# Optimization experiments

Measured on AMD Instinct MI355X. Metric: run time of the kernel, lower is better.

Reference implementation:

```python
import jax, jax.numpy as jnp
import numpy as np
import math

DIM = 256
HEADS = 8
DIM_HEAD = 64
INNER = HEADS * DIM_HEAD  # 512
WIN = 8
STRIDE = 4
W = 32          # patch_w_num
N = W * W       # 1024 tokens
B = 64
SCALE = DIM_HEAD ** -0.5


def setup_inputs() -> dict:
    key = jax.random.key(0)
    ks = jax.random.split(key, 6)
    return {
        "x": jax.random.normal(ks[0], (B, N, DIM), jnp.float32),
        "w_qkv": jax.random.normal(ks[1], (DIM, 3 * INNER), jnp.float32) * 0.02,
        "w_pro": jax.random.normal(ks[2], (3 * INNER, 3 * INNER), jnp.float32) * 0.02,
        "b_pro": jnp.zeros((3 * INNER,), jnp.float32),
        "w_out": jax.random.normal(ks[3], (INNER, DIM), jnp.float32) * 0.02,
        "b_out": jnp.zeros((DIM,), jnp.float32),
    }


def _window_ranges(stride):
    # Replicates window_split's static range construction (Python ints only).
    edges = list(range(-WIN, W + 1, WIN))
    pairs = list(zip(edges[:-1], edges[1:]))
    ranges = []
    for (i0, i1) in pairs:
        for (j0, j1) in pairs:
            r = [min(max(v + stride, 0), W) for v in (i0, j0, i1, j1)]
            if r[2] != r[0] and r[3] != r[1]:
                ranges.append(r)
    return ranges


def _cal_window(q, k, v, stride):
    # q,k,v: [b, h, n, d]
    b, h, n, d = q.shape
    ranges = _window_ranges(stride)
    S = WIN * WIN

    def split(t):
        t5 = t.reshape(b, h, W, W, d)
        blks = []
        for r0, c0, r1, c1 in ranges:
            blk = t5[:, :, r0:r1, c0:c1, :].reshape(b, h, -1, d)
            pad = S - blk.shape[2]
            blk = jnp.pad(blk, ((0, 0), (0, 0), (0, pad), (0, 0)))
            blks.append(blk)
        return jnp.stack(blks, axis=0)  # [nb, b, h, S, d]

    qs, ks_, vs = split(q), split(k), split(v)
    # NOTE: softmax runs over padded (zero) keys too, faithful to the source.
    dots = jnp.einsum('nbhid,nbhjd->nbhij', qs, ks_) * SCALE
    attn = jax.nn.softmax(dots, axis=-1)
    out = jnp.einsum('nbhij,nbhjd->nbhid', attn, vs)  # [nb, b, h, S, d]

    # window_merge: stitch variable-size blocks back into [b, h, W, W, d]
    h_count = int(math.sqrt(len(ranges)))
    rows = []
    for i in range(0, len(ranges), h_count):
        row = []
        for j in range(h_count):
            r0, c0, r1, c1 = ranges[i + j]
            num = (r1 - r0) * (c1 - c0)
            row.append(out[i + j, :, :, :num, :].reshape(b, h, r1 - r0, c1 - c0, d))
        rows.append(jnp.concatenate(row, axis=3))
    full = jnp.concatenate(rows, axis=2)  # [b, h, W, W, d]
    # 'b h num_h num_w d -> b (num_h num_w) (h d)'
    return full.transpose(0, 2, 3, 1, 4).reshape(b, W * W, h * d)


def reference(x, w_qkv, w_pro, b_pro, w_out, b_out):
    qkv = x @ w_qkv                                   # [b, n, 3*inner]
    qkv = jax.nn.gelu(qkv, approximate=False) @ w_pro + b_pro
    q, k, v = jnp.split(qkv, 3, axis=-1)

    def to_heads(t):
        bb, nn_ = t.shape[0], t.shape[1]
        return t.reshape(bb, nn_, HEADS, DIM_HEAD).transpose(0, 2, 1, 3)

    q, k, v = to_heads(q), to_heads(k), to_heads(v)
    outs = [_cal_window(q, k, v, s) for s in range(0, WIN, STRIDE)]
    out = jnp.mean(jnp.stack(outs, axis=-1), axis=-1)  # [b, n, inner]
    return out @ w_out + b_out
```

## Files before the change

### kernel.cpp

```cpp
#include <hip/hip_runtime.h>
#include <hip/hip_bf16.h>
#include <stdint.h>


#define TILE 64
#define BKK  32

typedef short bf16x8 __attribute__((ext_vector_type(8)));
typedef float f32x4 __attribute__((ext_vector_type(4)));

__device__ __forceinline__ unsigned short f2bf(float f) {
    unsigned u = __float_as_uint(f);
    return (unsigned short)((u + 0x7fffu + ((u >> 16) & 1u)) >> 16);
}

__device__ __forceinline__ float gelu_exact(float v) {
    return 0.5f * v * (1.0f + erff(v * 0.70710678118654752f));
}

__global__ __launch_bounds__(256) void conv_bf16(const float* __restrict__ src,
                                                 unsigned short* __restrict__ dst, int n4) {
    int i = blockIdx.x * 256 + threadIdx.x;
    const int stride = gridDim.x * 256;
    for (; i < n4; i += stride) {
        float4 v = reinterpret_cast<const float4*>(src)[i];
        ushort4 o;
        o.x = f2bf(v.x); o.y = f2bf(v.y); o.z = f2bf(v.z); o.w = f2bf(v.w);
        reinterpret_cast<ushort4*>(dst)[i] = o;
    }
}

__global__ __launch_bounds__(256) void transpose_bf16(const float* __restrict__ w,
                                                      unsigned short* __restrict__ wT,
                                                      int K, int N) {
    __shared__ float t[32][33];
    const int kb = blockIdx.y * 32, nb = blockIdx.x * 32;
    const int r = threadIdx.x >> 5, c = threadIdx.x & 31;
    #pragma unroll
    for (int i = 0; i < 4; ++i)
        t[r + i * 8][c] = w[(size_t)(kb + r + i * 8) * N + nb + c];
    __syncthreads();
    #pragma unroll
    for (int i = 0; i < 4; ++i)
        wT[(size_t)(nb + r + i * 8) * K + kb + c] = f2bf(t[c][r + i * 8]);
}

template<bool GELU, bool BIAS, bool OUTBF>
__global__ __launch_bounds__(256) void gemm_mfma(
    const unsigned short* __restrict__ A,
    const unsigned short* __restrict__ BT,
    const float* __restrict__ bias,
    void* __restrict__ Cv, int M, int N, int K, int nbx)
{
    __shared__ __align__(16) short lA[128 * BKK];
    __shared__ __align__(16) short lB[128 * BKK];
    const int tid  = threadIdx.x;
    const int lane = tid & 63;
    const int wid  = tid >> 6;

    const int cpx = gridDim.x >> 3;
    const int wg  = (blockIdx.x & 7) * cpx + (blockIdx.x >> 3);
    const int nb  = wg % nbx, mb = wg / nbx;

    const size_t bm = (size_t)mb * 128;
    const size_t bn = (size_t)nb * 128;

    const int wr = wid >> 1, wc = wid & 1;
    const int mr = wr * 64, nr = wc * 64;

    f32x4 acc[4][4] = {};

    const int srow = lane >> 2;
    const int sk8  = lane & 3;

    for (int k0 = 0; k0 < K; k0 += BKK) {
        #pragma unroll
        for (int s = 0; s < 2; ++s) {
            const int i = wid * 2 + s;
            const int row = i * 16 + srow;
            const unsigned short* ga = A  + (bm + row) * (size_t)K + k0 + sk8 * 8;
            const unsigned short* gb = BT + (bn + row) * (size_t)K + k0 + sk8 * 8;
            __builtin_amdgcn_global_load_lds(
                (const __attribute__((address_space(1))) unsigned int*)ga,
                (__attribute__((address_space(3))) unsigned int*)(lA + i * 512), 16, 0, 0);
            __builtin_amdgcn_global_load_lds(
                (const __attribute__((address_space(1))) unsigned int*)gb,
                (__attribute__((address_space(3))) unsigned int*)(lB + i * 512), 16, 0, 0);
        }
        __syncthreads();

        const int fr = lane & 15;
        const int fk = (lane >> 4) * 8;
        bf16x8 af[4], bq[4];
        #pragma unroll
        for (int m = 0; m < 4; ++m)
            af[m] = *reinterpret_cast<const bf16x8*>(&lA[(mr + m * 16 + fr) * BKK + fk]);
        #pragma unroll
        for (int n = 0; n < 4; ++n)
            bq[n] = *reinterpret_cast<const bf16x8*>(&lB[(nr + n * 16 + fr) * BKK + fk]);
        #pragma unroll
        for (int m = 0; m < 4; ++m)
            #pragma unroll
            for (int n = 0; n < 4; ++n)
                acc[m][n] = __builtin_amdgcn_mfma_f32_16x16x32_bf16(af[m], bq[n], acc[m][n], 0, 0, 0);
        __syncthreads();
    }

    const int fr = lane & 15;
    const int fq = lane >> 4;
    #pragma unroll
    for (int n = 0; n < 4; ++n) {
        const size_t col = bn + nr + n * 16 + fr;
        const float bv = BIAS ? bias[col] : 0.0f;
        #pragma unroll
        for (int m = 0; m < 4; ++m) {
            const size_t rbase = bm + mr + m * 16 + fq * 4;
            f32x4 a = acc[m][n];
            #pragma unroll
            for (int j = 0; j < 4; ++j) {
                float v = a[j] + bv;
                if (GELU) v = gelu_exact(v);
                if (OUTBF)
                    ((unsigned short*)Cv)[(rbase + j) * (size_t)N + col] = f2bf(v);
                else
                    ((float*)Cv)[(rbase + j) * (size_t)N + col] = v;
            }
        }
    }
}

template<bool GELU, bool BIAS, bool MEANA>
__global__ __launch_bounds__(256) void gemm_f32(
    const float* __restrict__ A, const float* __restrict__ A2,
    const float* __restrict__ B, const float* __restrict__ bias,
    float* __restrict__ C, int M, int N, int K)
{
    __shared__ __align__(16) float As[BKK][TILE + 4];
    __shared__ __align__(16) float Bs[BKK][TILE + 4];
    const int tid = threadIdx.x;
    const int tx = tid & 15;
    const int ty = tid >> 4;
    const long bm = (long)blockIdx.y * TILE;
    const long bn = (long)blockIdx.x * TILE;

    float acc[4][4] = {};

    for (int k0 = 0; k0 < K; k0 += BKK) {
        #pragma unroll
        for (int i = 0; i < 2; ++i) {
            int f4  = tid + i * 256;
            int row = f4 >> 3;
            int kk  = (f4 & 7) << 2;
            float4 a = *reinterpret_cast<const float4*>(A + (bm + row) * (long)K + k0 + kk);
            if (MEANA) {
                float4 a2 = *reinterpret_cast<const float4*>(A2 + (bm + row) * (long)K + k0 + kk);
                a.x = 0.5f * (a.x + a2.x); a.y = 0.5f * (a.y + a2.y);
                a.z = 0.5f * (a.z + a2.z); a.w = 0.5f * (a.w + a2.w);
            }
            As[kk + 0][row] = a.x; As[kk + 1][row] = a.y;
            As[kk + 2][row] = a.z; As[kk + 3][row] = a.w;
        }
        #pragma unroll
        for (int i = 0; i < 2; ++i) {
            int f4   = tid + i * 256;
            int krow = f4 >> 4;
            int nn   = (f4 & 15) << 2;
            *reinterpret_cast<float4*>(&Bs[krow][nn]) =
                *reinterpret_cast<const float4*>(B + (long)(k0 + krow) * N + bn + nn);
        }
        __syncthreads();
        #pragma unroll
        for (int kk = 0; kk < BKK; ++kk) {
            float4 av = *reinterpret_cast<const float4*>(&As[kk][ty << 2]);
            float4 bv = *reinterpret_cast<const float4*>(&Bs[kk][tx << 2]);
            float a_[4] = {av.x, av.y, av.z, av.w};
            float b_[4] = {bv.x, bv.y, bv.z, bv.w};
            #pragma unroll
            for (int u = 0; u < 4; ++u)
                #pragma unroll
                for (int w = 0; w < 4; ++w)
                    acc[u][w] = fmaf(a_[u], b_[w], acc[u][w]);
        }
        __syncthreads();
    }

    #pragma unroll
    for (int u = 0; u < 4; ++u) {
        long row = bm + (ty << 2) + u;
        float vals[4];
        #pragma unroll
        for (int w = 0; w < 4; ++w) {
            float v = acc[u][w];
            if (BIAS) v += bias[bn + (tx << 2) + w];
            if (GELU) v = gelu_exact(v);
            vals[w] = v;
        }
        *reinterpret_cast<float4*>(C + row * (long)N + bn + (tx << 2)) =
            make_float4(vals[0], vals[1], vals[2], vals[3]);
    }
}

__global__ __launch_bounds__(256) void attn_win(
    const float* __restrict__ qkvp, float* __restrict__ out0, float* __restrict__ out4)
{
    __shared__ __align__(16) float qT[64][68];
    __shared__ __align__(16) float kT[64][68];
    __shared__ __align__(16) float vS[64][68];
    __shared__ float pS[64][66];
    __shared__ float invS[64];

    const int widx = blockIdx.x;
    const int h    = blockIdx.y;
    const int b    = blockIdx.z;
    const int tid  = threadIdx.x;

    int r0, c0, nr, nc;
    float* outbuf;
    if (widx < 16) {
        r0 = (widx >> 2) << 3; c0 = (widx & 3) << 3;
        nr = 8; nc = 8;
        outbuf = out0;
    } else {
        int w  = widx - 16;
        int ri = w / 5, ci = w % 5;
        r0 = (ri == 0) ? 0 : (8 * ri - 4);
        nr = (ri == 0 || ri == 4) ? 4 : 8;
        c0 = (ci == 0) ? 0 : (8 * ci - 4);
        nc = (ci == 0 || ci == 4) ? 4 : 8;
        outbuf = out4;
    }
    const int num = nr * nc;
    const int ncl = (nc == 8) ? 3 : 2;
    const size_t tokbase = (size_t)b * 1024;

    for (int f4 = tid; f4 < num * 16; f4 += 256) {
        int t  = f4 >> 4;
        int d4 = (f4 & 15) << 2;
        int n  = ((r0 + (t >> ncl)) << 5) + c0 + (t & (nc - 1));
        const float* base = qkvp + (tokbase + n) * 1536 + h * 64 + d4;
        float4 qv = *reinterpret_cast<const float4*>(base);
        float4 kv = *reinterpret_cast<const float4*>(base + 512);
        float4 vv = *reinterpret_cast<const float4*>(base + 1024);
        qT[d4 + 0][t] = qv.x; qT[d4 + 1][t] = qv.y; qT[d4 + 2][t] = qv.z; qT[d4 + 3][t] = qv.w;
        kT[d4 + 0][t] = kv.x; kT[d4 + 1][t] = kv.y; kT[d4 + 2][t] = kv.z; kT[d4 + 3][t] = kv.w;
        *reinterpret_cast<float4*>(&vS[t][d4]) = vv;
    }
    __syncthreads();

    const int i0 = (tid >> 4) << 2;
    const int j0 = (tid & 15) << 2;
    if (i0 < num && j0 < num) {
        float acc[4][4] = {};
        #pragma unroll 16
        for (int d = 0; d < 64; ++d) {
            float4 qv = *reinterpret_cast<const float4*>(&qT[d][i0]);
            float4 kv = *reinterpret_cast<const float4*>(&kT[d][j0]);
            float q_[4] = {qv.x, qv.y, qv.z, qv.w};
            float k_[4] = {kv.x, kv.y, kv.z, kv.w};
            #pragma unroll
            for (int u = 0; u < 4; ++u)
                #pragma unroll
                for (int w = 0; w < 4; ++w)
                    acc[u][w] = fmaf(q_[u], k_[w], acc[u][w]);
        }
        #pragma unroll
        for (int u = 0; u < 4; ++u)
            #pragma unroll
            for (int w = 0; w < 4; ++w)
                pS[i0 + u][j0 + w] = acc[u][w] * 0.125f;
    }
    __syncthreads();

    if (tid < num) {
        const int i = tid;
        float m = (num < 64) ? 0.0f : -3.4e38f;
        for (int j = 0; j < num; ++j) m = fmaxf(m, pS[i][j]);
        float s = (float)(64 - num) * __expf(-m);
        for (int j = 0; j < num; ++j) {
            float e = __expf(pS[i][j] - m);
            pS[i][j] = e;
            s += e;
        }
        invS[i] = 1.0f / s;
    }
    __syncthreads();

    const int d0 = j0;
    if (i0 < num) {
        float acc[4][4] = {};
        #pragma unroll 8
        for (int j = 0; j < num; ++j) {
            float4 vv = *reinterpret_cast<const float4*>(&vS[j][d0]);
            float v_[4] = {vv.x, vv.y, vv.z, vv.w};
            float p_[4];
            #pragma unroll
            for (int u = 0; u < 4; ++u) p_[u] = pS[i0 + u][j];
            #pragma unroll
            for (int u = 0; u < 4; ++u)
                #pragma unroll
                for (int w = 0; w < 4; ++w)
                    acc[u][w] = fmaf(p_[u], v_[w], acc[u][w]);
        }
        #pragma unroll
        for (int u = 0; u < 4; ++u) {
            int t = i0 + u;
            int n = ((r0 + (t >> ncl)) << 5) + c0 + (t & (nc - 1));
            float inv = invS[t];
            *reinterpret_cast<float4*>(outbuf + (tokbase + n) * 512 + h * 64 + d0) =
                make_float4(acc[u][0] * inv, acc[u][1] * inv, acc[u][2] * inv, acc[u][3] * inv);
        }
    }
}

extern "C" void kernel_launch(void* const* d_in, const int* in_sizes, int n_in,
                              void* d_out, int out_size, void* d_ws, size_t ws_size,
                              hipStream_t stream) {
    const float* x     = (const float*)d_in[0];
    const float* w_qkv = (const float*)d_in[1];
    const float* w_pro = (const float*)d_in[2];
    const float* b_pro = (const float*)d_in[3];
    const float* w_out = (const float*)d_in[4];
    const float* b_out = (const float*)d_in[5];
    float* out = (float*)d_out;

    const int B = 64;
    const size_t WQKVT = 1536 * 256 * 2;
    const size_t WPROT = 1536 * 1536 * 2;
    const size_t PERB  = 1024 * (256 * 2 + 1536 * 2 + 1536 * 4 + 512 * 4 + 512 * 4);
    int CB = 16;
    while (CB > 1 && WQKVT + WPROT + (size_t)CB * PERB > ws_size) CB >>= 1;
    const int NCHUNK = B / CB;
    const int CM = CB * 1024;

    char* w8 = (char*)d_ws;
    unsigned short* wqkvT = (unsigned short*)w8;
    unsigned short* wproT = (unsigned short*)(w8 + WQKVT);
    char* cbase = w8 + WQKVT + WPROT;
    unsigned short* xb     = (unsigned short*)cbase;
    unsigned short* gelu_b = (unsigned short*)(cbase + (size_t)CM * 512);
    float*          qkvp   = (float*)(cbase + (size_t)CM * 512 + (size_t)CM * 3072);
    float*          att0   = (float*)((char*)qkvp + (size_t)CM * 6144);
    float*          att4   = (float*)((char*)att0 + (size_t)CM * 2048);

    dim3 blk(256);

    transpose_bf16<<<dim3(1536 / 32, 256 / 32), blk, 0, stream>>>(w_qkv, wqkvT, 256, 1536);
    transpose_bf16<<<dim3(1536 / 32, 1536 / 32), blk, 0, stream>>>(w_pro, wproT, 1536, 1536);

    const int nbx = 12;
    const int gg  = (CM / 128) * nbx;

    for (int c = 0; c < NCHUNK; ++c) {
        const size_t tok0 = (size_t)c * CM;
        conv_bf16<<<512, blk, 0, stream>>>(x + tok0 * 256, xb, CM * 256 / 4);
        gemm_mfma<true, false, true><<<gg, blk, 0, stream>>>(
            xb, wqkvT, nullptr, gelu_b, CM, 1536, 256, nbx);
        gemm_mfma<false, true, false><<<gg, blk, 0, stream>>>(
            gelu_b, wproT, b_pro, qkvp, CM, 1536, 1536, nbx);
        attn_win<<<dim3(41, 8, CB), blk, 0, stream>>>(qkvp, att0, att4);
        gemm_f32<false, true, true><<<dim3(256 / TILE, CM / TILE), blk, 0, stream>>>(
            att0, att4, w_out, b_out, out + tok0 * 256, CM, 256, 512);
    }
}
```

Before: 1.497 ms.

## Store qkv and attention outputs in bf16 and run output projection on MFMA

The pro-projection GEMM now writes bf16 instead of fp32, and the window-attention kernel reads bf16 and writes bf16 into one concatenated buffer holding both stride outputs. The mean of the two outputs is folded into a doubled, halved, transposed w_out (K=1024), so the final projection runs on the bf16 MFMA GEMM rather than the fp32 SIMT GEMM. This roughly halves intermediate memory traffic and moves the last GEMM onto matrix cores, at the cost of extra bf16 rounding on q/k/v and attention outputs.

After: 1.330 ms. -11.2%, faster.

```diff
diff --git a/kernel.cpp b/kernel.cpp
--- a/kernel.cpp
+++ b/kernel.cpp
@@ -3,8 +3,7 @@
 #include <stdint.h>
 
 
-#define TILE 64
-#define BKK  32
+#define BKK 32
 
 typedef short bf16x8 __attribute__((ext_vector_type(8)));
 typedef float f32x4 __attribute__((ext_vector_type(4)));
@@ -13,7 +12,9 @@
     unsigned u = __float_as_uint(f);
     return (unsigned short)((u + 0x7fffu + ((u >> 16) & 1u)) >> 16);
 }
-
+__device__ __forceinline__ float bf2f(unsigned short u) {
+    return __uint_as_float((unsigned)u << 16);
+}
 __device__ __forceinline__ float gelu_exact(float v) {
     return 0.5f * v * (1.0f + erff(v * 0.70710678118654752f));
 }
@@ -43,6 +44,24 @@
     #pragma unroll
     for (int i = 0; i < 4; ++i)
         wT[(size_t)(nb + r + i * 8) * K + kb + c] = f2bf(t[c][r + i * 8]);
+}
+
+__global__ __launch_bounds__(256) void make_w4T(const float* __restrict__ w,
+                                                unsigned short* __restrict__ w4T) {
+    __shared__ float t[32][33];
+    const int kb = blockIdx.y * 32, nb = blockIdx.x * 32;
+    const int r = threadIdx.x >> 5, c = threadIdx.x & 31;
+    #pragma unroll
+    for (int i = 0; i < 4; ++i)
+        t[r + i * 8][c] = w[(size_t)(kb + r + i * 8) * 256 + nb + c];
+    __syncthreads();
+    #pragma unroll
+    for (int i = 0; i < 4; ++i) {
+        unsigned short v = f2bf(0.5f * t[c][r + i * 8]);
+        size_t n = nb + r + i * 8, k = kb + c;
+        w4T[n * 1024 + k]       = v;
+        w4T[n * 1024 + 512 + k] = v;
+    }
 }
 
 template<bool GELU, bool BIAS, bool OUTBF>
@@ -129,79 +148,8 @@
     }
 }
 
-template<bool GELU, bool BIAS, bool MEANA>
-__global__ __launch_bounds__(256) void gemm_f32(
-    const float* __restrict__ A, const float* __restrict__ A2,
-    const float* __restrict__ B, const float* __restrict__ bias,
-    float* __restrict__ C, int M, int N, int K)
-{
-    __shared__ __align__(16) float As[BKK][TILE + 4];
-    __shared__ __align__(16) float Bs[BKK][TILE + 4];
-    const int tid = threadIdx.x;
-    const int tx = tid & 15;
-    const int ty = tid >> 4;
-    const long bm = (long)blockIdx.y * TILE;
-    const long bn = (long)blockIdx.x * TILE;
-
-    float acc[4][4] = {};
-
-    for (int k0 = 0; k0 < K; k0 += BKK) {
-        #pragma unroll
-        for (int i = 0; i < 2; ++i) {
-            int f4  = tid + i * 256;
-            int row = f4 >> 3;
-            int kk  = (f4 & 7) << 2;
-            float4 a = *reinterpret_cast<const float4*>(A + (bm + row) * (long)K + k0 + kk);
-            if (MEANA) {
-                float4 a2 = *reinterpret_cast<const float4*>(A2 + (bm + row) * (long)K + k0 + kk);
-                a.x = 0.5f * (a.x + a2.x); a.y = 0.5f * (a.y + a2.y);
-                a.z = 0.5f * (a.z + a2.z); a.w = 0.5f * (a.w + a2.w);
-            }
-            As[kk + 0][row] = a.x; As[kk + 1][row] = a.y;
-            As[kk + 2][row] = a.z; As[kk + 3][row] = a.w;
-        }
-        #pragma unroll
-        for (int i = 0; i < 2; ++i) {
-            int f4   = tid + i * 256;
-            int krow = f4 >> 4;
-            int nn   = (f4 & 15) << 2;
-            *reinterpret_cast<float4*>(&Bs[krow][nn]) =
-                *reinterpret_cast<const float4*>(B + (long)(k0 + krow) * N + bn + nn);
-        }
-        __syncthreads();
-        #pragma unroll
-        for (int kk = 0; kk < BKK; ++kk) {
-            float4 av = *reinterpret_cast<const float4*>(&As[kk][ty << 2]);
-            float4 bv = *reinterpret_cast<const float4*>(&Bs[kk][tx << 2]);
-            float a_[4] = {av.x, av.y, av.z, av.w};
-            float b_[4] = {bv.x, bv.y, bv.z, bv.w};
-            #pragma unroll
-            for (int u = 0; u < 4; ++u)
-                #pragma unroll
-                for (int w = 0; w < 4; ++w)
-                    acc[u][w] = fmaf(a_[u], b_[w], acc[u][w]);
-        }
-        __syncthreads();
-    }
-
-    #pragma unroll
-    for (int u = 0; u < 4; ++u) {
-        long row = bm + (ty << 2) + u;
-        float vals[4];
-        #pragma unroll
-        for (int w = 0; w < 4; ++w) {
-            float v = acc[u][w];
-            if (BIAS) v += bias[bn + (tx << 2) + w];
-            if (GELU) v = gelu_exact(v);
-            vals[w] = v;
-        }
-        *reinterpret_cast<float4*>(C + row * (long)N + bn + (tx << 2)) =
-            make_float4(vals[0], vals[1], vals[2], vals[3]);
-    }
-}
-
 __global__ __launch_bounds__(256) void attn_win(
-    const float* __restrict__ qkvp, float* __restrict__ out0, float* __restrict__ out4)
+    const unsigned short* __restrict__ qkvp, unsigned short* __restrict__ attc)
 {
     __shared__ __align__(16) float qT[64][68];
     __shared__ __align__(16) float kT[64][68];
@@ -214,12 +162,10 @@
     const int b    = blockIdx.z;
     const int tid  = threadIdx.x;
 
-    int r0, c0, nr, nc;
-    float* outbuf;
+    int r0, c0, nr, nc, sOff;
     if (widx < 16) {
         r0 = (widx >> 2) << 3; c0 = (widx & 3) << 3;
-        nr = 8; nc = 8;
-        outbuf = out0;
+        nr = 8; nc = 8; sOff = 0;
     } else {
         int w  = widx - 16;
         int ri = w / 5, ci = w % 5;
@@ -227,7 +173,7 @@
         nr = (ri == 0 || ri == 4) ? 4 : 8;
         c0 = (ci == 0) ? 0 : (8 * ci - 4);
         nc = (ci == 0 || ci == 4) ? 4 : 8;
-        outbuf = out4;
+        sOff = 512;
     }
     const int num = nr * nc;
     const int ncl = (nc == 8) ? 3 : 2;
@@ -237,13 +183,16 @@
         int t  = f4 >> 4;
         int d4 = (f4 & 15) << 2;
         int n  = ((r0 + (t >> ncl)) << 5) + c0 + (t & (nc - 1));
-        const float* base = qkvp + (tokbase + n) * 1536 + h * 64 + d4;
-        float4 qv = *reinterpret_cast<const float4*>(base);
-        float4 kv = *reinterpret_cast<const float4*>(base + 512);
-        float4 vv = *reinterpret_cast<const float4*>(base + 1024);
-        qT[d4 + 0][t] = qv.x; qT[d4 + 1][t] = qv.y; qT[d4 + 2][t] = qv.z; qT[d4 + 3][t] = qv.w;
-        kT[d4 + 0][t] = kv.x; kT[d4 + 1][t] = kv.y; kT[d4 + 2][t] = kv.z; kT[d4 + 3][t] = kv.w;
-        *reinterpret_cast<float4*>(&vS[t][d4]) = vv;
+        const unsigned short* base = qkvp + (tokbase + n) * 1536 + h * 64 + d4;
+        ushort4 qv = *reinterpret_cast<const ushort4*>(base);
+        ushort4 kv = *reinterpret_cast<const ushort4*>(base + 512);
+        ushort4 vv = *reinterpret_cast<const ushort4*>(base + 1024);
+        qT[d4 + 0][t] = bf2f(qv.x); qT[d4 + 1][t] = bf2f(qv.y);
+        qT[d4 + 2][t] = bf2f(qv.z); qT[d4 + 3][t] = bf2f(qv.w);
+        kT[d4 + 0][t] = bf2f(kv.x); kT[d4 + 1][t] = bf2f(kv.y);
+        kT[d4 + 2][t] = bf2f(kv.z); kT[d4 + 3][t] = bf2f(kv.w);
+        vS[t][d4 + 0] = bf2f(vv.x); vS[t][d4 + 1] = bf2f(vv.y);
+        vS[t][d4 + 2] = bf2f(vv.z); vS[t][d4 + 3] = bf2f(vv.w);
     }
     __syncthreads();
 
@@ -306,8 +255,10 @@
             int t = i0 + u;
             int n = ((r0 + (t >> ncl)) << 5) + c0 + (t & (nc - 1));
             float inv = invS[t];
-            *reinterpret_cast<float4*>(outbuf + (tokbase + n) * 512 + h * 64 + d0) =
-                make_float4(acc[u][0] * inv, acc[u][1] * inv, acc[u][2] * inv, acc[u][3] * inv);
+            ushort4 o;
+            o.x = f2bf(acc[u][0] * inv); o.y = f2bf(acc[u][1] * inv);
+            o.z = f2bf(acc[u][2] * inv); o.w = f2bf(acc[u][3] * inv);
+            *reinterpret_cast<ushort4*>(attc + (tokbase + n) * 1024 + sOff + h * 64 + d0) = o;
         }
     }
 }
@@ -326,39 +277,42 @@
     const int B = 64;
     const size_t WQKVT = 1536 * 256 * 2;
     const size_t WPROT = 1536 * 1536 * 2;
-    const size_t PERB  = 1024 * (256 * 2 + 1536 * 2 + 1536 * 4 + 512 * 4 + 512 * 4);
+    const size_t W4T   = 256 * 1024 * 2;
+    const size_t PERB  = 1024 * (256 * 2 + 1536 * 2 + 1536 * 2 + 1024 * 2);
     int CB = 16;
-    while (CB > 1 && WQKVT + WPROT + (size_t)CB * PERB > ws_size) CB >>= 1;
+    while (CB > 1 && WQKVT + WPROT + W4T + (size_t)CB * PERB > ws_size) CB >>= 1;
     const int NCHUNK = B / CB;
     const int CM = CB * 1024;
 
     char* w8 = (char*)d_ws;
     unsigned short* wqkvT = (unsigned short*)w8;
     unsigned short* wproT = (unsigned short*)(w8 + WQKVT);
-    char* cbase = w8 + WQKVT + WPROT;
+    unsigned short* w4T   = (unsigned short*)(w8 + WQKVT + WPROT);
+    char* cbase = w8 + WQKVT + WPROT + W4T;
     unsigned short* xb     = (unsigned short*)cbase;
     unsigned short* gelu_b = (unsigned short*)(cbase + (size_t)CM * 512);
-    float*          qkvp   = (float*)(cbase + (size_t)CM * 512 + (size_t)CM * 3072);
-    float*          att0   = (float*)((char*)qkvp + (size_t)CM * 6144);
-    float*          att4   = (float*)((char*)att0 + (size_t)CM * 2048);
+    unsigned short* qkvp_b = (unsigned short*)(cbase + (size_t)CM * 512 + (size_t)CM * 3072);
+    unsigned short* attc   = (unsigned short*)((char*)qkvp_b + (size_t)CM * 3072);
 
     dim3 blk(256);
 
     transpose_bf16<<<dim3(1536 / 32, 256 / 32), blk, 0, stream>>>(w_qkv, wqkvT, 256, 1536);
     transpose_bf16<<<dim3(1536 / 32, 1536 / 32), blk, 0, stream>>>(w_pro, wproT, 1536, 1536);
-
-    const int nbx = 12;
-    const int gg  = (CM / 128) * nbx;
+    make_w4T<<<dim3(256 / 32, 512 / 32), blk, 0, stream>>>(w_out, w4T);
+
+    const int nbx12 = 12;
+    const int gg    = (CM / 128) * nbx12;
+    const int gg4   = (CM / 128) * 2;
 
     for (int c = 0; c < NCHUNK; ++c) {
         const size_t tok0 = (size_t)c * CM;
         conv_bf16<<<512, blk, 0, stream>>>(x + tok0 * 256, xb, CM * 256 / 4);
         gemm_mfma<true, false, true><<<gg, blk, 0, stream>>>(
-            xb, wqkvT, nullptr, gelu_b, CM, 1536, 256, nbx);
-        gemm_mfma<false, true, false><<<gg, blk, 0, stream>>>(
-            gelu_b, wproT, b_pro, qkvp, CM, 1536, 1536, nbx);
-        attn_win<<<dim3(41, 8, CB), blk, 0, stream>>>(qkvp, att0, att4);
-        gemm_f32<false, true, true><<<dim3(256 / TILE, CM / TILE), blk, 0, stream>>>(
-            att0, att4, w_out, b_out, out + tok0 * 256, CM, 256, 512);
-    }
-}
+            xb, wqkvT, nullptr, gelu_b, CM, 1536, 256, nbx12);
+        gemm_mfma<false, true, true><<<gg, blk, 0, stream>>>(
+            gelu_b, wproT, b_pro, qkvp_b, CM, 1536, 1536, nbx12);
+        attn_win<<<dim3(41, 8, CB), blk, 0, stream>>>(qkvp_b, attc);
+        gemm_mfma<false, true, false><<<gg4, blk, 0, stream>>>(
+            attc, w4T, b_out, out + tok0 * 256, CM, 256, 1024, 2);
+    }
+}
```
